# Performance work log

Hardware: AMD Instinct MI355X
Metric: run time of the kernel (lower is better)

## Reference

```python
import jax, jax.numpy as jnp
import numpy as np

R = 4            # num_runs
P_DROP = 0.2     # node dropout prob
BN_EPS = 1e-5
L = 2            # num_layers
D = 128          # hidden_channels
NA, NP_ = 50000, 100000
E = 500000


def setup_inputs() -> dict:
    key = jax.random.key(0)
    ks = jax.random.split(key, 20)
    s = 0.05
    x_author = jax.random.normal(ks[0], (NA, D), jnp.float32)
    x_paper = jax.random.normal(ks[1], (NP_, D), jnp.float32)
    # edge_index rows: [src, dst]
    ei_ap = jnp.stack([
        jax.random.randint(ks[2], (E,), 0, NA),
        jax.random.randint(ks[3], (E,), 0, NP_)]).astype(jnp.int64)
    ei_pa = jnp.stack([
        jax.random.randint(ks[4], (E,), 0, NP_),
        jax.random.randint(ks[5], (E,), 0, NA)]).astype(jnp.int64)
    # bernoulli(1-p) keep masks, one per run per node
    drop_author = (jax.random.uniform(ks[6], (R, NA)) < (1.0 - P_DROP)).astype(jnp.float32)
    drop_paper = (jax.random.uniform(ks[7], (R, NP_)) < (1.0 - P_DROP)).astype(jnp.float32)
    return {
        "x_author": x_author, "x_paper": x_paper,
        "ei_ap": ei_ap, "ei_pa": ei_pa,
        "drop_author": drop_author, "drop_paper": drop_paper,
        "lin_a_w": jax.random.normal(ks[8], (D, D)) * s,
        "lin_a_b": jnp.zeros((D,), jnp.float32),
        "lin_p_w": jax.random.normal(ks[9], (D, D)) * s,
        "lin_p_b": jnp.zeros((D,), jnp.float32),
        "W1": jax.random.normal(ks[10], (L, 2, D, D)) * s,
        "B1": jnp.zeros((L, 2, D), jnp.float32),
        "G": jnp.ones((L, 2, D), jnp.float32),
        "BT": jnp.zeros((L, 2, D), jnp.float32),
        "W2": jax.random.normal(ks[11], (L, 2, D, D)) * s,
        "B2": jnp.zeros((L, 2, D), jnp.float32),
        "EPS": jnp.zeros((L, 2), jnp.float32),  # GIN train_eps init 0
        "final_w": jax.random.normal(ks[12], (D, 4)) * s,
        "final_b": jnp.zeros((4,), jnp.float32),
    }


def _gin(x_src, x_dst, ei, eps, w1, b1, g, bt, w2, b2):
    # x_src: [Rs*Ns, D] flattened over runs; x_dst: [Rd*Nd, D]
    # scatter-sum neighbor messages into dst (only run-0 slots touched,
    # matching the original code which reuses the unexpanded edge_index)
    agg = jnp.zeros_like(x_dst).at[ei[1]].add(x_src[ei[0]])
    z = (1.0 + eps) * x_dst + agg
    h = z @ w1 + b1
    # BatchNorm1d, training-mode batch stats (biased variance)
    mu = h.mean(axis=0)
    var = ((h - mu) ** 2).mean(axis=0)
    h = (h - mu) * jax.lax.rsqrt(var + BN_EPS) * g + bt
    h = jax.nn.relu(h)
    return h @ w2 + b2


def reference(x_author, x_paper, ei_ap, ei_pa, drop_author, drop_paper,
              lin_a_w, lin_a_b, lin_p_w, lin_p_b,
              W1, B1, G, BT, W2, B2, EPS, final_w, final_b):
    inv_keep = 1.0 / (1.0 - P_DROP)
    # input projections, expand over runs, DropGNN node dropout
    h_a = x_author @ lin_a_w + lin_a_b                       # [Na, D]
    h_a = jnp.broadcast_to(h_a[None], (R,) + h_a.shape)      # [R, Na, D]
    h_a = h_a * drop_author[..., None] * inv_keep
    h_p = x_paper @ lin_p_w + lin_p_b
    h_p = jnp.broadcast_to(h_p[None], (R,) + h_p.shape)
    h_p = h_p * drop_paper[..., None] * inv_keep

    for l in range(L):
        xa = h_a.reshape(-1, D)
        xp = h_p.reshape(-1, D)
        # edge type 0: author -writes-> paper ; edge type 1: paper -> author
        new_p = _gin(xa, xp, ei_ap, EPS[l, 0], W1[l, 0], B1[l, 0], G[l, 0], BT[l, 0], W2[l, 0], B2[l, 0])
        new_a = _gin(xp, xa, ei_pa, EPS[l, 1], W1[l, 1], B1[l, 1], G[l, 1], BT[l, 1], W2[l, 1], B2[l, 1])
        h_a = jax.nn.relu(new_a.reshape(R, NA, D))
        h_p = jax.nn.relu(new_p.reshape(R, NP_, D))

    h = h_a.mean(axis=0)                                     # [Na, D]
    return h @ final_w + final_b                             # [Na, num_classes]
```

## Files before the change

kernel.cpp:

```cpp
#include <hip/hip_runtime.h>

#define NRUNS 4
#define NAU 50000
#define NPP 100000
#define NEDGE 500000
#define HD 128
#define INV_KEEP 1.25f
#define BN_EPS 1e-5f
#define LDA 136
#define NB_GEMM 1024

#define M_PROJ   0
#define M_GIN1   1
#define M_GIN2   2
#define M_PROJ1  3
#define M_GIN1M  4

#define C_AP ((NPP + 1023) / 1024)
#define C_PA ((NAU + 1023) / 1024)

typedef unsigned short bf16r;
typedef __attribute__((ext_vector_type(8))) short v8s;
typedef __attribute__((ext_vector_type(4))) float v4f;

__device__ inline float bf2f(bf16r u) {
    return __uint_as_float(((unsigned)u) << 16);
}
__device__ inline bf16r f2bf(float f) {
    __bf16 b = (__bf16)f;
    return __builtin_bit_cast(bf16r, b);
}

__global__ __launch_bounds__(256)
void zero_k(float* p, long n4) {
    long i = (long)blockIdx.x * 256 + threadIdx.x;
    long stride = (long)gridDim.x * 256;
    float4 z = make_float4(0.f, 0.f, 0.f, 0.f);
    for (; i < n4; i += stride) ((float4*)p)[i] = z;
}

__global__ __launch_bounds__(256)
void convw_prep_k(const float* __restrict__ lin_a_w, const float* __restrict__ lin_p_w,
                  const float* __restrict__ W1, const float* __restrict__ W2,
                  bf16r* __restrict__ wt, float* __restrict__ stats,
                  float* __restrict__ curz, int curz4)
{
    int b = blockIdx.x;
    if (b < 640) {
        int t = b >> 6;
        int e = (b & 63) * 256 + threadIdx.x;
        const float* src;
        if (t == 0) src = lin_a_w;
        else if (t == 1) src = lin_p_w;
        else if (t < 6) src = W1 + (size_t)(t - 2) * HD * HD;
        else src = W2 + (size_t)(t - 6) * HD * HD;
        int n = e >> 7, k = e & 127;
        wt[(size_t)t * HD * HD + e] = f2bf(src[(size_t)k * HD + n]);
    } else if (b == 640) {
        ((float4*)stats)[threadIdx.x] = make_float4(0.f, 0.f, 0.f, 0.f);
    } else {
        int i = (b - 641) * 256 + threadIdx.x;
        if (i < curz4) ((float4*)curz)[i] = make_float4(0.f, 0.f, 0.f, 0.f);
    }
}

__global__ __launch_bounds__(256)
void count2_k(const int* __restrict__ ei_ap, const int* __restrict__ ei_pa,
              int* curA, int* curB)
{
    int g = blockIdx.x * 256 + threadIdx.x;
    if (g < NEDGE) atomicAdd(&curA[ei_ap[NEDGE + g]], 1);
    else if (g < 2 * NEDGE) atomicAdd(&curB[ei_pa[NEDGE + (g - NEDGE)]], 1);
}

__global__ __launch_bounds__(256)
void scan1m_k(const int* __restrict__ curA, int* offA,
              const int* __restrict__ curB, int* offB, int* partial)
{
    __shared__ int lds[256];
    int b = blockIdx.x, t = threadIdx.x;
    const int* in; int* out; int n, chunk;
    if (b < C_AP) { in = curA; out = offA; n = NPP; chunk = b; }
    else          { in = curB; out = offB; n = NAU; chunk = b - C_AP; }
    int base = chunk * 1024 + t * 4;
    int v0 = 0, v1 = 0, v2 = 0, v3 = 0;
    if (base + 3 < n) {
        int4 x = *(const int4*)(in + base);
        v0 = x.x; v1 = x.y; v2 = x.z; v3 = x.w;
    } else {
        if (base + 0 < n) v0 = in[base + 0];
        if (base + 1 < n) v1 = in[base + 1];
        if (base + 2 < n) v2 = in[base + 2];
        if (base + 3 < n) v3 = in[base + 3];
    }
    int s = v0 + v1 + v2 + v3;
    lds[t] = s;
    __syncthreads();
    for (int d = 1; d < 256; d <<= 1) {
        int x = (t >= d) ? lds[t - d] : 0;
        __syncthreads();
        lds[t] += x;
        __syncthreads();
    }
    int excl = lds[t] - s;
    if (base + 0 < n) out[base + 0] = excl;
    if (base + 1 < n) out[base + 1] = excl + v0;
    if (base + 2 < n) out[base + 2] = excl + v0 + v1;
    if (base + 3 < n) out[base + 3] = excl + v0 + v1 + v2;
    if (t == 255) partial[b] = lds[255];
}

__global__ __launch_bounds__(256)
void scan2m_k(int* partial)
{
    __shared__ int lds[256];
    int t = threadIdx.x;
    int base = blockIdx.x == 0 ? 0 : C_AP;
    int n = blockIdx.x == 0 ? C_AP : C_PA;
    int s = (t < n) ? partial[base + t] : 0;
    lds[t] = s;
    __syncthreads();
    for (int d = 1; d < 256; d <<= 1) {
        int x = (t >= d) ? lds[t - d] : 0;
        __syncthreads();
        lds[t] += x;
        __syncthreads();
    }
    if (t < n) partial[base + t] = lds[t] - s;
}

__global__ __launch_bounds__(256)
void scan3m_k(int* offA, int* curA, int* offB, int* curB,
              const int* __restrict__ partial)
{
    int b = blockIdx.x, t = threadIdx.x;
    int* off; int* cur; int n, chunk;
    if (b < C_AP) { off = offA; cur = curA; n = NPP; chunk = b; }
    else          { off = offB; cur = curB; n = NAU; chunk = b - C_AP; }
    int add = partial[b];
    int base = chunk * 1024 + t * 4;
    #pragma unroll
    for (int j = 0; j < 4; ++j) {
        int i = base + j;
        if (i < n) {
            int v = off[i] + add;
            off[i] = v;
            cur[i] = v;
        }
    }
    if (chunk == 0 && t == 0) off[n] = NEDGE;
}

__global__ __launch_bounds__(256)
void fill2_k(const int* __restrict__ ei_ap, const int* __restrict__ ei_pa,
             int* curA, int* bktA, int* curB, int* bktB)
{
    int g = blockIdx.x * 256 + threadIdx.x;
    if (g < NEDGE) {
        int d = ei_ap[NEDGE + g];
        bktA[atomicAdd(&curA[d], 1)] = ei_ap[g];
    } else if (g < 2 * NEDGE) {
        int e = g - NEDGE;
        int d = ei_pa[NEDGE + e];
        bktB[atomicAdd(&curB[d], 1)] = ei_pa[e];
    }
}

template<bool MASKED>
__global__ __launch_bounds__(256)
void gather2_k(const bf16r* __restrict__ hA, const bf16r* __restrict__ hP,
               bf16r* __restrict__ aggP, bf16r* __restrict__ aggA,
               const int* __restrict__ offAP, const int* __restrict__ bktAP,
               const int* __restrict__ offPA, const int* __restrict__ bktPA,
               const float* __restrict__ mA0, const float* __restrict__ mP0)
{
    int gw = (blockIdx.x * 256 + threadIdx.x) >> 6;
    int lane = threadIdx.x & 63;
    const bf16r* src; bf16r* agg; const int* off; const int* bkt;
    const float* msk; int w;
    if (gw < NPP) { src = hA; agg = aggP; off = offAP; bkt = bktAP; msk = mA0; w = gw; }
    else          { src = hP; agg = aggA; off = offPA; bkt = bktPA; msk = mP0; w = gw - NPP; }
    int s0 = off[w], s1 = off[w + 1];
    float a0 = 0.f, a1 = 0.f;
    int e = s0;
    for (; e + 1 < s1; e += 2) {
        int i0 = bkt[e], i1 = bkt[e + 1];
        ushort2 u = *(const ushort2*)(src + (size_t)i0 * HD + lane * 2);
        ushort2 v = *(const ushort2*)(src + (size_t)i1 * HD + lane * 2);
        if constexpr (MASKED) {
            float m0 = msk[i0] * INV_KEEP, m1 = msk[i1] * INV_KEEP;
            a0 += m0 * bf2f(u.x) + m1 * bf2f(v.x);
            a1 += m0 * bf2f(u.y) + m1 * bf2f(v.y);
        } else {
            a0 += bf2f(u.x) + bf2f(v.x);
            a1 += bf2f(u.y) + bf2f(v.y);
        }
    }
    if (e < s1) {
        int i0 = bkt[e];
        ushort2 u = *(const ushort2*)(src + (size_t)i0 * HD + lane * 2);
        float m0 = MASKED ? msk[i0] * INV_KEEP : 1.0f;
        a0 += m0 * bf2f(u.x);
        a1 += m0 * bf2f(u.y);
    }
    ushort2 o;
    o.x = f2bf(a0);
    o.y = f2bf(a1);
    *(ushort2*)(agg + (size_t)w * HD + lane * 2) = o;
}

__global__ __launch_bounds__(256)
void scatter_k(const bf16r* __restrict__ src, float* dst,
               const int* __restrict__ ei, int E)
{
    int g = blockIdx.x * 256 + threadIdx.x;
    int e = g >> 5, lane = g & 31;
    if (e >= E) return;
    int s = ei[e], d = ei[E + e];
    ushort4 u = *(const ushort4*)(src + (size_t)s * HD + lane * 4);
    float* dp = dst + (size_t)d * HD + lane * 4;
    unsafeAtomicAdd(dp + 0, bf2f(u.x));
    unsafeAtomicAdd(dp + 1, bf2f(u.y));
    unsafeAtomicAdd(dp + 2, bf2f(u.z));
    unsafeAtomicAdd(dp + 3, bf2f(u.w));
}

struct SideP {
    const void* in;
    bf16r* out;
    const void* agg;
    const bf16r* wt;
    const float* bias;
    const float* epsp;
    float* gsum;
    float* gsumsq;
    const float* gamma;
    const float* beta;
    float invN;
    const float* mask;
    int M, Nn, tiles;
};

template<int MODE, typename IT, typename AT>
__global__ __launch_bounds__(512)
void mfma_gemm(SideP P, SideP A, int BP)
{
    __shared__ bf16r za[64][LDA];
    __shared__ float red[2][HD];
    const int tid = threadIdx.x;

    SideP S;
    int t, tstride;
    if ((int)blockIdx.x < BP) { S = P; t = blockIdx.x; tstride = BP; }
    else { S = A; t = (int)blockIdx.x - BP; tstride = NB_GEMM - BP; }
    if (t >= S.tiles) return;

    constexpr bool GIN1ANY = (MODE == M_GIN1 || MODE == M_GIN1M);
    constexpr bool PMSK    = (MODE == M_GIN1M);
    constexpr int  NVH     = (MODE == M_PROJ || MODE == M_PROJ1) ? 2 : 1;
    constexpr int  NVA     = (GIN1ANY && sizeof(AT) == 4) ? 2 : 1;

    const int wid = tid >> 6, lane = tid & 63;
    const int lr = lane & 15, lk = (lane >> 4) * 8;
    const int colq = (lane >> 4) * 4;
    const int cb = wid * 16;
    const int srow = tid >> 4;
    const int scol = (tid & 15) * 8;

    float epsv = 1.0f;
    if (GIN1ANY) epsv = 1.0f + S.epsp[0];

    v8s w[4];
    #pragma unroll
    for (int ks = 0; ks < 4; ++ks)
        w[ks] = *(const v8s*)(S.wt + (size_t)(cb + lr) * HD + ks * 32 + lk);

    const float4 bb = *(const float4*)(S.bias + cb + colq);

    float sc8[MODE == M_GIN2 ? 8 : 1], sh8[MODE == M_GIN2 ? 8 : 1];
    if constexpr (MODE == M_GIN2) {
        #pragma unroll
        for (int j = 0; j < 8; ++j) {
            int c = scol + j;
            float mu = S.gsum[c] * S.invN;
            float var = S.gsumsq[c] * S.invN - mu * mu;
            float s = S.gamma[c] * rsqrtf(var + BN_EPS);
            sc8[j] = s;
            sh8[j] = S.beta[c] - mu * s;
        }
    }

    float st_s[4], st_q[4];
    if (GIN1ANY) {
        #pragma unroll
        for (int j = 0; j < 4; ++j) { st_s[j] = 0.f; st_q[j] = 0.f; }
    }

    int4 pre[2][NVH];
    int4 preA[2][NVA];
    float mpre[PMSK ? 2 : 1];

    auto prefetch = [&](int tt) {
        int m0n = tt * 64;
        #pragma unroll
        for (int i = 0; i < 2; ++i) {
            int gr = m0n + srow + 32 * i;
            if constexpr (PMSK) {
                int run = (gr >= S.Nn) + (gr >= 2 * S.Nn) + (gr >= 3 * S.Nn);
                int node = gr - run * S.Nn;
                mpre[i] = S.mask[gr];
                pre[i][0] = *(const int4*)((const bf16r*)S.in + (size_t)node * HD + scol);
            } else if (gr < S.M) {
                const int4* p = (const int4*)((const IT*)S.in + (size_t)gr * HD + scol);
                pre[i][0] = p[0];
                if constexpr (NVH == 2) pre[i][1] = p[1];
            } else {
                pre[i][0] = make_int4(0, 0, 0, 0);
                if constexpr (NVH == 2) pre[i][1] = make_int4(0, 0, 0, 0);
            }
            if constexpr (GIN1ANY) {
                if (gr < S.Nn) {
                    const int4* pa = (const int4*)((const AT*)S.agg + (size_t)gr * HD + scol);
                    preA[i][0] = pa[0];
                    if constexpr (NVA == 2) preA[i][1] = pa[1];
                } else {
                    preA[i][0] = make_int4(0, 0, 0, 0);
                    if constexpr (NVA == 2) preA[i][1] = make_int4(0, 0, 0, 0);
                }
            }
        }
    };

    prefetch(t);

    for (;;) {
        const int m0 = t * 64;
        #pragma unroll
        for (int i = 0; i < 2; ++i) {
            int row = srow + 32 * i;
            float v[8];
            if constexpr (NVH == 2) {
                const float* pf = (const float*)&pre[i][0];
                #pragma unroll
                for (int j = 0; j < 8; ++j) v[j] = pf[j];
            } else {
                const bf16r* pu = (const bf16r*)&pre[i][0];
                #pragma unroll
                for (int j = 0; j < 8; ++j) v[j] = bf2f(pu[j]);
            }
            if constexpr (GIN1ANY) {
                float av[8];
                if constexpr (sizeof(AT) == 4) {
                    const float* pa = (const float*)&preA[i][0];
                    #pragma unroll
                    for (int j = 0; j < 8; ++j) av[j] = pa[j];
                } else {
                    const bf16r* pa = (const bf16r*)&preA[i][0];
                    #pragma unroll
                    for (int j = 0; j < 8; ++j) av[j] = bf2f(pa[j]);
                }
                float coef = epsv;
                if constexpr (PMSK) coef = mpre[i] * INV_KEEP * epsv;
                #pragma unroll
                for (int j = 0; j < 8; ++j) v[j] = v[j] * coef + av[j];
            } else if constexpr (MODE == M_GIN2) {
                #pragma unroll
                for (int j = 0; j < 8; ++j)
                    v[j] = fmaxf(v[j] * sc8[j] + sh8[j], 0.f);
            }
            union { v8s w8; bf16r u[8]; } pk;
            #pragma unroll
            for (int j = 0; j < 8; ++j) pk.u[j] = f2bf(v[j]);
            *(v8s*)&za[row][scol] = pk.w8;
        }
        __syncthreads();

        const int tn = t + tstride;
        const bool more = tn < S.tiles;
        if (more) prefetch(tn);

        v4f acc[4];
        #pragma unroll
        for (int rf = 0; rf < 4; ++rf) acc[rf] = (v4f){0.f, 0.f, 0.f, 0.f};

        #pragma unroll
        for (int ks = 0; ks < 4; ++ks)
            #pragma unroll
            for (int rf = 0; rf < 4; ++rf) {
                v8s a = *(const v8s*)&za[rf * 16 + lr][ks * 32 + lk];
                acc[rf] = __builtin_amdgcn_mfma_f32_16x16x32_bf16(w[ks], a, acc[rf], 0, 0, 0);
            }

        #pragma unroll
        for (int rf = 0; rf < 4; ++rf) {
            acc[rf][0] += bb.x; acc[rf][1] += bb.y;
            acc[rf][2] += bb.z; acc[rf][3] += bb.w;
        }

        if constexpr (MODE == M_PROJ) {
            #pragma unroll
            for (int rf = 0; rf < 4; ++rf) {
                int grow = m0 + rf * 16 + lr;
                if (grow < S.M) {
                    #pragma unroll
                    for (int run = 0; run < NRUNS; ++run) {
                        float wm = S.mask[(size_t)run * S.Nn + grow] * INV_KEEP;
                        ushort4 o;
                        o.x = f2bf(acc[rf][0] * wm);
                        o.y = f2bf(acc[rf][1] * wm);
                        o.z = f2bf(acc[rf][2] * wm);
                        o.w = f2bf(acc[rf][3] * wm);
                        *(ushort4*)(S.out + ((size_t)run * S.Nn + grow) * HD + cb + colq) = o;
                    }
                }
            }
        } else if constexpr (MODE == M_PROJ1) {
            #pragma unroll
            for (int rf = 0; rf < 4; ++rf) {
                int grow = m0 + rf * 16 + lr;
                if (grow < S.M) {
                    ushort4 o;
                    o.x = f2bf(acc[rf][0]);
                    o.y = f2bf(acc[rf][1]);
                    o.z = f2bf(acc[rf][2]);
                    o.w = f2bf(acc[rf][3]);
                    *(ushort4*)(S.out + (size_t)grow * HD + cb + colq) = o;
                }
            }
        } else if constexpr (GIN1ANY) {
            #pragma unroll
            for (int rf = 0; rf < 4; ++rf) {
                int grow = m0 + rf * 16 + lr;
                ushort4 o;
                o.x = f2bf(acc[rf][0]);
                o.y = f2bf(acc[rf][1]);
                o.z = f2bf(acc[rf][2]);
                o.w = f2bf(acc[rf][3]);
                *(ushort4*)(S.out + (size_t)grow * HD + cb + colq) = o;
            }
            #pragma unroll
            for (int j = 0; j < 4; ++j)
                #pragma unroll
                for (int rf = 0; rf < 4; ++rf) {
                    float vv = acc[rf][j];
                    st_s[j] += vv;
                    st_q[j] += vv * vv;
                }
        } else {
            #pragma unroll
            for (int rf = 0; rf < 4; ++rf) {
                int grow = m0 + rf * 16 + lr;
                ushort4 o;
                o.x = f2bf(fmaxf(acc[rf][0], 0.f));
                o.y = f2bf(fmaxf(acc[rf][1], 0.f));
                o.z = f2bf(fmaxf(acc[rf][2], 0.f));
                o.w = f2bf(fmaxf(acc[rf][3], 0.f));
                *(ushort4*)(S.out + (size_t)grow * HD + cb + colq) = o;
            }
        }

        if (!more) break;
        t = tn;
        __syncthreads();
    }

    if constexpr (GIN1ANY) {
        #pragma unroll
        for (int d = 1; d < 16; d <<= 1)
            #pragma unroll
            for (int j = 0; j < 4; ++j) {
                st_s[j] += __shfl_xor(st_s[j], d);
                st_q[j] += __shfl_xor(st_q[j], d);
            }
        if (lr == 0) {
            #pragma unroll
            for (int j = 0; j < 4; ++j) {
                red[0][cb + colq + j] = st_s[j];
                red[1][cb + colq + j] = st_q[j];
            }
        }
        __syncthreads();
        if (tid < HD) {
            unsafeAtomicAdd(S.gsum + tid, red[0][tid]);
            unsafeAtomicAdd(S.gsumsq + tid, red[1][tid]);
        }
    }
}

__global__ __launch_bounds__(256)
void final_k(const bf16r* __restrict__ ha, const float* __restrict__ fw,
             const float* __restrict__ fb, float* __restrict__ out)
{
    int g = blockIdx.x * 256 + threadIdx.x;
    int node = g >> 6, lane = g & 63;
    if (node >= NAU) return;
    float m0 = 0.f, m1 = 0.f;
    #pragma unroll
    for (int r = 0; r < NRUNS; ++r) {
        size_t base = ((size_t)r * NAU + node) * HD;
        m0 += bf2f(ha[base + lane]);
        m1 += bf2f(ha[base + 64 + lane]);
    }
    m0 *= 0.25f;
    m1 *= 0.25f;
    float p[4];
    #pragma unroll
    for (int c = 0; c < 4; ++c)
        p[c] = m0 * fw[lane * 4 + c] + m1 * fw[(lane + 64) * 4 + c];
    #pragma unroll
    for (int off = 32; off >= 1; off >>= 1)
        #pragma unroll
        for (int c = 0; c < 4; ++c) p[c] += __shfl_down(p[c], off);
    if (lane == 0) {
        #pragma unroll
        for (int c = 0; c < 4; ++c) out[(size_t)node * 4 + c] = p[c] + fb[c];
    }
}

#define CSR_INTS ((size_t)(NPP + 4) + NEDGE + (NAU + 4) + NEDGE)
#define WT_ELEMS ((size_t)10 * HD * HD)

template<bool GATHER>
static void run_all(void* const* d_in, void* d_out, void* d_ws, hipStream_t stream)
{
    const float* x_author = (const float*)d_in[0];
    const float* x_paper  = (const float*)d_in[1];
    const int*   ei_ap    = (const int*)d_in[2];
    const int*   ei_pa    = (const int*)d_in[3];
    const float* drop_a   = (const float*)d_in[4];
    const float* drop_p   = (const float*)d_in[5];
    const float* lin_a_w  = (const float*)d_in[6];
    const float* lin_a_b  = (const float*)d_in[7];
    const float* lin_p_w  = (const float*)d_in[8];
    const float* lin_p_b  = (const float*)d_in[9];
    const float* W1       = (const float*)d_in[10];
    const float* B1       = (const float*)d_in[11];
    const float* G        = (const float*)d_in[12];
    const float* BT       = (const float*)d_in[13];
    const float* W2       = (const float*)d_in[14];
    const float* B2       = (const float*)d_in[15];
    const float* EPS      = (const float*)d_in[16];
    const float* fw       = (const float*)d_in[17];
    const float* fb       = (const float*)d_in[18];

    float* stats = (float*)d_ws;
    bf16r* wt = (bf16r*)(stats + 8 * HD);
    char* cp = (char*)(wt + WT_ELEMS);

    int *off_ap = nullptr, *bkt_ap = nullptr, *off_pa = nullptr, *bkt_pa = nullptr;
    if (GATHER) {
        int* ip = (int*)cp;
        off_ap = ip;  ip += NPP + 4;
        bkt_ap = ip;  ip += NEDGE;
        off_pa = ip;  ip += NAU + 4;
        bkt_pa = ip;  ip += NEDGE;
        cp = (char*)ip;
    }
    void* agg_a_v = cp;
    size_t aggElem = GATHER ? sizeof(bf16r) : sizeof(float);
    void* agg_p_v = cp + (size_t)NAU * HD * aggElem;
    cp += (size_t)(NAU + NPP) * HD * aggElem;
    bf16r* proj_a = nullptr; bf16r* proj_p = nullptr;
    if (GATHER) {
        proj_a = (bf16r*)cp;  cp += (size_t)NAU * HD * sizeof(bf16r);
        proj_p = (bf16r*)cp;  cp += (size_t)NPP * HD * sizeof(bf16r);
    }
    bf16r* h_a = (bf16r*)cp;
    bf16r* h_p = h_a + (size_t)NRUNS * NAU * HD;

    const bf16r* wt_lin_a = wt;
    const bf16r* wt_lin_p = wt + (size_t)1 * HD * HD;
    const bf16r* wt_W1    = wt + (size_t)2 * HD * HD;
    const bf16r* wt_W2    = wt + (size_t)6 * HD * HD;

    int* cur_ap = (int*)agg_a_v;
    int* cur_pa = cur_ap + NPP;
    int* partial = cur_pa + NAU;

    convw_prep_k<<<788, 256, 0, stream>>>(lin_a_w, lin_p_w, W1, W2, wt, stats,
                                          (float*)cur_ap, (NPP + NAU) / 4);

    if (GATHER) {
        count2_k<<<(2 * NEDGE + 255) / 256, 256, 0, stream>>>(ei_ap, ei_pa, cur_ap, cur_pa);
        scan1m_k<<<C_AP + C_PA, 256, 0, stream>>>(cur_ap, off_ap, cur_pa, off_pa, partial);
        scan2m_k<<<2, 256, 0, stream>>>(partial);
        scan3m_k<<<C_AP + C_PA, 256, 0, stream>>>(off_ap, cur_ap, off_pa, cur_pa, partial);
        fill2_k<<<(2 * NEDGE + 255) / 256, 256, 0, stream>>>(ei_ap, ei_pa,
                                                             cur_ap, bkt_ap, cur_pa, bkt_pa);
    }

    const int TP = NRUNS * NPP / 64, TA = NRUNS * NAU / 64;
    const int BPgin = (int)((long)NB_GEMM * TP / (TP + TA));

    if (GATHER) {
        SideP Pp = {}, Pa = {};
        Pp.in = x_paper; Pp.out = proj_p; Pp.wt = wt_lin_p; Pp.bias = lin_p_b;
        Pp.M = NPP; Pp.Nn = NPP; Pp.tiles = (NPP + 63) / 64;
        Pa.in = x_author; Pa.out = proj_a; Pa.wt = wt_lin_a; Pa.bias = lin_a_b;
        Pa.M = NAU; Pa.Nn = NAU; Pa.tiles = (NAU + 63) / 64;
        int BPproj = (int)((long)NB_GEMM * Pp.tiles / (Pp.tiles + Pa.tiles));
        mfma_gemm<M_PROJ1, float, float><<<NB_GEMM, 512, 0, stream>>>(Pp, Pa, BPproj);

        for (int l = 0; l < 2; ++l) {
            int t0 = l * 2 + 0, t1 = l * 2 + 1;

            if (l == 0) {
                gather2_k<true><<<((NPP + NAU) * 64) / 256, 256, 0, stream>>>(
                    proj_a, proj_p, (bf16r*)agg_p_v, (bf16r*)agg_a_v,
                    off_ap, bkt_ap, off_pa, bkt_pa, drop_a, drop_p);
            } else {
                gather2_k<false><<<((NPP + NAU) * 64) / 256, 256, 0, stream>>>(
                    h_a, h_p, (bf16r*)agg_p_v, (bf16r*)agg_a_v,
                    off_ap, bkt_ap, off_pa, bkt_pa, nullptr, nullptr);
            }

            SideP G1p = {}, G1a = {};
            G1p.wt = wt_W1 + (size_t)t0 * HD * HD;
            G1p.bias = B1 + (size_t)t0 * HD; G1p.epsp = EPS + t0;
            G1p.agg = agg_p_v;
            G1p.gsum = stats + t0 * 2 * HD; G1p.gsumsq = G1p.gsum + HD;
            G1p.M = NRUNS * NPP; G1p.Nn = NPP; G1p.tiles = TP; G1p.out = h_p;
            G1a.wt = wt_W1 + (size_t)t1 * HD * HD;
            G1a.bias = B1 + (size_t)t1 * HD; G1a.epsp = EPS + t1;
            G1a.agg = agg_a_v;
            G1a.gsum = stats + t1 * 2 * HD; G1a.gsumsq = G1a.gsum + HD;
            G1a.M = NRUNS * NAU; G1a.Nn = NAU; G1a.tiles = TA; G1a.out = h_a;
            if (l == 0) {
                G1p.in = proj_p; G1p.mask = drop_p;
                G1a.in = proj_a; G1a.mask = drop_a;
                mfma_gemm<M_GIN1M, bf16r, bf16r><<<NB_GEMM, 512, 0, stream>>>(G1p, G1a, BPgin);
            } else {
                G1p.in = h_p;
                G1a.in = h_a;
                mfma_gemm<M_GIN1, bf16r, bf16r><<<NB_GEMM, 512, 0, stream>>>(G1p, G1a, BPgin);
            }

            SideP G2p = {}, G2a = {};
            G2p.in = h_p; G2p.out = h_p; G2p.wt = wt_W2 + (size_t)t0 * HD * HD;
            G2p.bias = B2 + (size_t)t0 * HD;
            G2p.gsum = stats + t0 * 2 * HD; G2p.gsumsq = G2p.gsum + HD;
            G2p.gamma = G + (size_t)t0 * HD; G2p.beta = BT + (size_t)t0 * HD;
            G2p.invN = 1.0f / (NRUNS * NPP);
            G2p.M = NRUNS * NPP; G2p.Nn = NPP; G2p.tiles = TP;
            G2a.in = h_a; G2a.out = h_a; G2a.wt = wt_W2 + (size_t)t1 * HD * HD;
            G2a.bias = B2 + (size_t)t1 * HD;
            G2a.gsum = stats + t1 * 2 * HD; G2a.gsumsq = G2a.gsum + HD;
            G2a.gamma = G + (size_t)t1 * HD; G2a.beta = BT + (size_t)t1 * HD;
            G2a.invN = 1.0f / (NRUNS * NAU);
            G2a.M = NRUNS * NAU; G2a.Nn = NAU; G2a.tiles = TA;
            mfma_gemm<M_GIN2, bf16r, float><<<NB_GEMM, 512, 0, stream>>>(G2p, G2a, BPgin);
        }
    } else {
        SideP Pp = {}, Pa = {};
        Pp.in = x_paper; Pp.out = h_p; Pp.wt = wt_lin_p; Pp.bias = lin_p_b;
        Pp.mask = drop_p; Pp.M = NPP; Pp.Nn = NPP; Pp.tiles = (NPP + 63) / 64;
        Pa.in = x_author; Pa.out = h_a; Pa.wt = wt_lin_a; Pa.bias = lin_a_b;
        Pa.mask = drop_a; Pa.M = NAU; Pa.Nn = NAU; Pa.tiles = (NAU + 63) / 64;
        int BPproj = (int)((long)NB_GEMM * Pp.tiles / (Pp.tiles + Pa.tiles));
        mfma_gemm<M_PROJ, float, float><<<NB_GEMM, 512, 0, stream>>>(Pp, Pa, BPproj);

        for (int l = 0; l < 2; ++l) {
            int t0 = l * 2 + 0, t1 = l * 2 + 1;
            zero_k<<<2048, 256, 0, stream>>>((float*)agg_a_v, ((size_t)(NAU + NPP) * HD) / 4);
            scatter_k<<<(NEDGE * 32) / 256, 256, 0, stream>>>(h_a, (float*)agg_p_v, ei_ap, NEDGE);
            scatter_k<<<(NEDGE * 32) / 256, 256, 0, stream>>>(h_p, (float*)agg_a_v, ei_pa, NEDGE);

            SideP G1p = {}, G1a = {};
            G1p.in = h_p; G1p.out = h_p; G1p.wt = wt_W1 + (size_t)t0 * HD * HD;
            G1p.bias = B1 + (size_t)t0 * HD; G1p.agg = agg_p_v; G1p.epsp = EPS + t0;
            G1p.gsum = stats + t0 * 2 * HD; G1p.gsumsq = G1p.gsum + HD;
            G1p.M = NRUNS * NPP; G1p.Nn = NPP; G1p.tiles = TP;
            G1a.in = h_a; G1a.out = h_a; G1a.wt = wt_W1 + (size_t)t1 * HD * HD;
            G1a.bias = B1 + (size_t)t1 * HD; G1a.agg = agg_a_v; G1a.epsp = EPS + t1;
            G1a.gsum = stats + t1 * 2 * HD; G1a.gsumsq = G1a.gsum + HD;
            G1a.M = NRUNS * NAU; G1a.Nn = NAU; G1a.tiles = TA;
            mfma_gemm<M_GIN1, bf16r, float><<<NB_GEMM, 512, 0, stream>>>(G1p, G1a, BPgin);

            SideP G2p = {}, G2a = {};
            G2p.in = h_p; G2p.out = h_p;
            G2p.wt = wt_W2 + (size_t)t0 * HD * HD; G2p.bias = B2 + (size_t)t0 * HD;
            G2p.gsum = stats + t0 * 2 * HD; G2p.gsumsq = G2p.gsum + HD;
            G2p.gamma = G + (size_t)t0 * HD; G2p.beta = BT + (size_t)t0 * HD;
            G2p.invN = 1.0f / (NRUNS * NPP);
            G2p.M = NRUNS * NPP; G2p.Nn = NPP; G2p.tiles = TP;
            G2a.in = h_a; G2a.out = h_a;
            G2a.wt = wt_W2 + (size_t)t1 * HD * HD; G2a.bias = B2 + (size_t)t1 * HD;
            G2a.gsum = stats + t1 * 2 * HD; G2a.gsumsq = G2a.gsum + HD;
            G2a.gamma = G + (size_t)t1 * HD; G2a.beta = BT + (size_t)t1 * HD;
            G2a.invN = 1.0f / (NRUNS * NAU);
            G2a.M = NRUNS * NAU; G2a.Nn = NAU; G2a.tiles = TA;
            mfma_gemm<M_GIN2, bf16r, float><<<NB_GEMM, 512, 0, stream>>>(G2p, G2a, BPgin);
        }
    }

    final_k<<<(NAU * 64) / 256, 256, 0, stream>>>(h_a, fw, fb, (float*)d_out);
}

extern "C" void kernel_launch(void* const* d_in, const int* in_sizes, int n_in,
                              void* d_out, int out_size, void* d_ws, size_t ws_size,
                              hipStream_t stream)
{
    const size_t hB    = (size_t)NRUNS * (NAU + NPP) * HD * sizeof(bf16r);
    const size_t statB = 8 * HD * sizeof(float);
    const size_t wtB   = WT_ELEMS * sizeof(bf16r);
    const size_t csrB  = CSR_INTS * sizeof(int);
    const size_t aggBF = (size_t)(NAU + NPP) * HD * sizeof(bf16r);
    const size_t projB = (size_t)(NAU + NPP) * HD * sizeof(bf16r);

    const size_t need_gather = statB + wtB + csrB + aggBF + projB + hB;
    if (ws_size >= need_gather) {
        run_all<true>(d_in, d_out, d_ws, stream);
    } else {
        run_all<false>(d_in, d_out, d_ws, stream);
    }
}
```

Baseline: 579.0 us.

## Double-buffer GEMM LDS tile and unroll gather loop by four

The GEMM kernel now alternates between two LDS tile buffers, which lets it drop the trailing barrier at the end of each tile iteration. The next tile can be written while other waves still read the previous one. The gather kernel processes four edges per iteration with two independent accumulator pairs, putting more loads in flight and shortening the add dependency chain. The costs are doubled LDS use for the tile, which may reduce occupancy, and a slightly different floating-point summation order.

After: 563.5 us. 2.7% less time.

```diff
diff --git a/kernel.cpp b/kernel.cpp
--- a/kernel.cpp
+++ b/kernel.cpp
@@ -181,28 +181,33 @@
     if (gw < NPP) { src = hA; agg = aggP; off = offAP; bkt = bktAP; msk = mA0; w = gw; }
     else          { src = hP; agg = aggA; off = offPA; bkt = bktPA; msk = mP0; w = gw - NPP; }
     int s0 = off[w], s1 = off[w + 1];
-    float a0 = 0.f, a1 = 0.f;
+    float a0 = 0.f, a1 = 0.f, b0 = 0.f, b1 = 0.f;
     int e = s0;
-    for (; e + 1 < s1; e += 2) {
-        int i0 = bkt[e], i1 = bkt[e + 1];
-        ushort2 u = *(const ushort2*)(src + (size_t)i0 * HD + lane * 2);
-        ushort2 v = *(const ushort2*)(src + (size_t)i1 * HD + lane * 2);
+    for (; e + 3 < s1; e += 4) {
+        int i0 = bkt[e], i1 = bkt[e + 1], i2 = bkt[e + 2], i3 = bkt[e + 3];
+        ushort2 u0 = *(const ushort2*)(src + (size_t)i0 * HD + lane * 2);
+        ushort2 u1 = *(const ushort2*)(src + (size_t)i1 * HD + lane * 2);
+        ushort2 u2 = *(const ushort2*)(src + (size_t)i2 * HD + lane * 2);
+        ushort2 u3 = *(const ushort2*)(src + (size_t)i3 * HD + lane * 2);
+        float m0 = 1.f, m1 = 1.f, m2 = 1.f, m3 = 1.f;
         if constexpr (MASKED) {
-            float m0 = msk[i0] * INV_KEEP, m1 = msk[i1] * INV_KEEP;
-            a0 += m0 * bf2f(u.x) + m1 * bf2f(v.x);
-            a1 += m0 * bf2f(u.y) + m1 * bf2f(v.y);
-        } else {
-            a0 += bf2f(u.x) + bf2f(v.x);
-            a1 += bf2f(u.y) + bf2f(v.y);
-        }
-    }
-    if (e < s1) {
+            m0 = msk[i0] * INV_KEEP; m1 = msk[i1] * INV_KEEP;
+            m2 = msk[i2] * INV_KEEP; m3 = msk[i3] * INV_KEEP;
+        }
+        a0 += m0 * bf2f(u0.x) + m1 * bf2f(u1.x);
+        a1 += m0 * bf2f(u0.y) + m1 * bf2f(u1.y);
+        b0 += m2 * bf2f(u2.x) + m3 * bf2f(u3.x);
+        b1 += m2 * bf2f(u2.y) + m3 * bf2f(u3.y);
+    }
+    for (; e < s1; ++e) {
         int i0 = bkt[e];
         ushort2 u = *(const ushort2*)(src + (size_t)i0 * HD + lane * 2);
         float m0 = MASKED ? msk[i0] * INV_KEEP : 1.0f;
         a0 += m0 * bf2f(u.x);
         a1 += m0 * bf2f(u.y);
     }
+    a0 += b0;
+    a1 += b1;
     ushort2 o;
     o.x = f2bf(a0);
     o.y = f2bf(a1);
@@ -245,7 +250,7 @@
 __global__ __launch_bounds__(512)
 void mfma_gemm(SideP P, SideP A, int BP)
 {
-    __shared__ bf16r za[64][LDA];
+    __shared__ bf16r za[2][64][LDA];
     __shared__ float red[2][HD];
     const int tid = threadIdx.x;
 
@@ -333,6 +338,7 @@
 
     prefetch(t);
 
+    int cur = 0;
     for (;;) {
         const int m0 = t * 64;
         #pragma unroll
@@ -371,7 +377,7 @@
             union { v8s w8; bf16r u[8]; } pk;
             #pragma unroll
             for (int j = 0; j < 8; ++j) pk.u[j] = f2bf(v[j]);
-            *(v8s*)&za[row][scol] = pk.w8;
+            *(v8s*)&za[cur][row][scol] = pk.w8;
         }
         __syncthreads();
 
@@ -387,7 +393,7 @@
         for (int ks = 0; ks < 4; ++ks)
             #pragma unroll
             for (int rf = 0; rf < 4; ++rf) {
-                v8s a = *(const v8s*)&za[rf * 16 + lr][ks * 32 + lk];
+                v8s a = *(const v8s*)&za[cur][rf * 16 + lr][ks * 32 + lk];
                 acc[rf] = __builtin_amdgcn_mfma_f32_16x16x32_bf16(w[ks], a, acc[rf], 0, 0, 0);
             }
 
@@ -461,7 +467,7 @@
 
         if (!more) break;
         t = tn;
-        __syncthreads();
+        cur ^= 1;
     }
 
     if constexpr (GIN1ANY) {
```
